# Performance work log

Measured on AMD Instinct MI355X. Metric: run time of the kernel, lower is better.

## Reference

```python
import jax, jax.numpy as jnp
import numpy as np

N = 25000        # nodes
E = 400000       # edges (avg degree 16)
F = 128          # num_features
NRBF = 20        # num_rbf_features
CUTOFF = 5.0


def setup_inputs() -> dict:
    key = jax.random.key(0)
    ks = jax.random.split(key, 9)
    node_scalar = jax.random.normal(ks[0], (N, F), jnp.float32)
    node_vector = jax.random.normal(ks[1], (N, F, 3), jnp.float32)
    dst = jax.random.randint(ks[2], (E,), 0, N)
    src = jax.random.randint(ks[3], (E,), 0, N)
    r = jax.random.normal(ks[4], (E, 3), jnp.float32) * 1.5
    d = jnp.clip(jnp.linalg.norm(r, axis=-1), 0.1, None)
    adj_matrix = jnp.concatenate(
        [dst[:, None].astype(jnp.float32), src[:, None].astype(jnp.float32), r, d[:, None]],
        axis=-1)  # [E, 6]
    s_in = 1.0 / np.sqrt(F)
    s_rbf = 1.0 / np.sqrt(NRBF)
    W1 = jax.random.normal(ks[5], (F, F), jnp.float32) * s_in
    b1 = jnp.zeros((F,), jnp.float32)
    W2 = jax.random.normal(ks[6], (F, 3 * F), jnp.float32) * s_in
    b2 = jnp.zeros((3 * F,), jnp.float32)
    Wr = jax.random.normal(ks[7], (NRBF, 3 * F), jnp.float32) * s_rbf
    br = jnp.zeros((3 * F,), jnp.float32)
    return dict(node_scalar=node_scalar, node_vector=node_vector, adj_matrix=adj_matrix,
                W1=W1, b1=b1, W2=W2, b2=b2, Wr=Wr, br=br)


def reference(node_scalar, node_vector, adj_matrix, W1, b1, W2, b2, Wr, br):
    # scalar message MLP: Linear -> SiLU -> Linear, [N, 3F]
    atom_scalar = jax.nn.silu(node_scalar @ W1 + b1) @ W2 + b2

    dst = adj_matrix[:, 0].astype(jnp.int32)
    src = adj_matrix[:, 1].astype(jnp.int32)
    r_ij = adj_matrix[:, 2:5]              # [E, 3]
    d = adj_matrix[:, 5]                   # [E]

    # sinc expansion: sin(d * n * pi / cutoff) / d, n = 1..NRBF -> [E, NRBF]
    n_vals = jnp.arange(1, NRBF + 1, dtype=jnp.float32)
    sinc = jnp.sin(d[:, None] * n_vals * jnp.pi / CUTOFF) / d[:, None]
    rbf = sinc @ Wr + br                   # [E, 3F]
    cut = jnp.where(d < CUTOFF, 0.5 * (jnp.cos(jnp.pi * d / CUTOFF) + 1.0), 0.0)
    w = rbf * cut[:, None]                 # [E, 3F]

    pre_split = atom_scalar[src] * w       # [E, 3F]
    s1, s2, s3 = jnp.split(pre_split, 3, axis=-1)  # each [E, F]

    r_hat = r_ij / d[:, None]              # [E, 3]
    # message_vector: [E, F, 3]
    message_vector = node_vector[src] * s1[:, :, None] + s3[:, :, None] * r_hat[:, None, :]

    delta_s = jnp.zeros_like(node_scalar).at[dst].add(s2)
    delta_v = jnp.zeros_like(node_vector).at[dst].add(message_vector)
    return node_scalar + delta_s, node_vector + delta_v
```

## Files before the change

kernel.cpp:

```cpp
#include <hip/hip_runtime.h>

#define FDIM 128
#define NRBF 20
constexpr float CUTOFF_F = 5.0f;
constexpr float PI_F = 3.14159265358979323846f;

typedef _Float16 h2 __attribute__((ext_vector_type(2)));

__device__ __forceinline__ uint packh(float a, float b) {
  union { _Float16 h[2]; uint u; } x;
  x.h[0] = (_Float16)a;
  x.h[1] = (_Float16)b;
  return x.u;
}
__device__ __forceinline__ float h_lo(uint w) {
  union { uint u; _Float16 h[2]; } x;
  x.u = w;
  return (float)x.h[0];
}
__device__ __forceinline__ float h_hi(uint w) {
  union { uint u; _Float16 h[2]; } x;
  x.u = w;
  return (float)x.h[1];
}
__device__ __forceinline__ ushort f2us(float f) {
  union { _Float16 h; ushort s; } x;
  x.h = (_Float16)f;
  return x.s;
}
__device__ __forceinline__ float dot2(uint cw, h2 w, float acc) {
#if __has_builtin(__builtin_amdgcn_fdot2)
  h2 c = __builtin_bit_cast(h2, cw);
  return __builtin_amdgcn_fdot2(c, w, acc, false);
#else
  return fmaf(h_hi(cw), (float)w[1], fmaf(h_lo(cw), (float)w[0], acc));
#endif
}

__global__ __launch_bounds__(256) void gemm_fused(
    const float* __restrict__ A, const float* __restrict__ W1,
    const float* __restrict__ b1, const float* __restrict__ W2,
    const float* __restrict__ b2, ushort* __restrict__ atomh, int M) {
  __shared__ float As[64][FDIM + 4];
  const int row0 = blockIdx.x * 64;
  const int t = threadIdx.x;
  const int tx = t & 15;
  const int ty = t >> 4;
  const int cl = tx * 8;
  const int r0 = ty * 4;

  for (int i = t; i < 64 * 32; i += 256) {
    int r = i >> 5;
    int cc = (i & 31) << 2;
    int gr = row0 + r;
    float4 v = make_float4(0.f, 0.f, 0.f, 0.f);
    if (gr < M) v = *(const float4*)&A[(size_t)gr * FDIM + cc];
    *(float4*)&As[r][cc] = v;
  }
  __syncthreads();

  float acc[4][8];
#pragma unroll
  for (int r = 0; r < 4; ++r)
#pragma unroll
    for (int c = 0; c < 8; ++c) acc[r][c] = 0.f;
#pragma unroll 4
  for (int k = 0; k < FDIM; ++k) {
    const float* wr = W1 + (size_t)k * FDIM + cl;
    float4 wa = *(const float4*)wr;
    float4 wb = *(const float4*)(wr + 4);
    float w[8] = {wa.x, wa.y, wa.z, wa.w, wb.x, wb.y, wb.z, wb.w};
    float a[4];
#pragma unroll
    for (int r = 0; r < 4; ++r) a[r] = As[r0 + r][k];
#pragma unroll
    for (int r = 0; r < 4; ++r)
#pragma unroll
      for (int c = 0; c < 8; ++c) acc[r][c] = fmaf(a[r], w[c], acc[r][c]);
  }
  float hv[4][8];
#pragma unroll
  for (int r = 0; r < 4; ++r)
#pragma unroll
    for (int c = 0; c < 8; ++c) {
      float x = acc[r][c] + b1[cl + c];
      hv[r][c] = x / (1.f + __expf(-x));
    }
  __syncthreads();
#pragma unroll
  for (int r = 0; r < 4; ++r)
#pragma unroll
    for (int c = 0; c < 8; ++c) As[r0 + r][cl + c] = hv[r][c];
  __syncthreads();

#pragma unroll 1
  for (int p = 0; p < 3; ++p) {
    const int c0 = p * 128 + cl;
#pragma unroll
    for (int r = 0; r < 4; ++r)
#pragma unroll
      for (int c = 0; c < 8; ++c) acc[r][c] = 0.f;
#pragma unroll 4
    for (int k = 0; k < FDIM; ++k) {
      const float* wr = W2 + (size_t)k * 384 + c0;
      float4 wa = *(const float4*)wr;
      float4 wb = *(const float4*)(wr + 4);
      float w[8] = {wa.x, wa.y, wa.z, wa.w, wb.x, wb.y, wb.z, wb.w};
      float a[4];
#pragma unroll
      for (int r = 0; r < 4; ++r) a[r] = As[r0 + r][k];
#pragma unroll
      for (int r = 0; r < 4; ++r)
#pragma unroll
        for (int c = 0; c < 8; ++c) acc[r][c] = fmaf(a[r], w[c], acc[r][c]);
    }
#pragma unroll
    for (int r = 0; r < 4; ++r) {
      int gr = row0 + r0 + r;
      if (gr >= M) continue;
      union { ushort s[8]; uint4 q; } pk;
#pragma unroll
      for (int c = 0; c < 8; ++c) pk.s[c] = f2us(acc[r][c] + b2[c0 + c]);
      *(uint4*)&atomh[(size_t)gr * 384 + c0] = pk.q;
    }
  }
}

__global__ __launch_bounds__(256) void pack_kernel(
    const ushort* __restrict__ atomh, const float* __restrict__ nvec,
    uint* __restrict__ bundle, int NF) {
  for (int i = blockIdx.x * blockDim.x + threadIdx.x; i < NF;
       i += gridDim.x * blockDim.x) {
    int n = i >> 7, j = i & 127;
    const ushort* ab = atomh + (size_t)n * 384;
    uint a0 = ab[j], a1 = ab[j + 128], a2 = ab[j + 256];
    const float* vb = nvec + (size_t)i * 3;
    uint* o = bundle + (size_t)i * 3;
    o[0] = a0 | (a1 << 16);
    o[1] = a2 | ((uint)f2us(vb[0]) << 16);
    o[2] = (uint)f2us(vb[1]) | ((uint)f2us(vb[2]) << 16);
  }
}

__global__ __launch_bounds__(256) void hist_kernel(const float* __restrict__ adj,
                                                   int* __restrict__ counts,
                                                   int E) {
  int e = blockIdx.x * blockDim.x + threadIdx.x;
  if (e < E) atomicAdd(&counts[(int)adj[(size_t)e * 6]], 1);
}

__global__ __launch_bounds__(1024) void scan_kernel(
    const int* __restrict__ counts, int* __restrict__ offs,
    int* __restrict__ cursor, int n) {
  __shared__ int part[1024];
  const int tid = threadIdx.x;
  const int CH = (n + 1023) >> 10;
  const int b = tid * CH;
  const int e = min(b + CH, n);
  int s = 0;
  for (int i = b; i < e; ++i) s += counts[i];
  part[tid] = s;
  __syncthreads();
  for (int off = 1; off < 1024; off <<= 1) {
    int v = (tid >= off) ? part[tid - off] : 0;
    __syncthreads();
    part[tid] += v;
    __syncthreads();
  }
  int run = part[tid] - s;
  if (tid == 0) offs[0] = 0;
  for (int i = b; i < e; ++i) {
    int c = counts[i];
    cursor[i] = run;
    run += c;
    offs[i + 1] = run;
  }
}

__global__ __launch_bounds__(256) void edge_prep(const float* __restrict__ adj,
                                                 int* __restrict__ cursor,
                                                 int* __restrict__ eids,
                                                 uint* __restrict__ rec, int E) {
  int e = blockIdx.x * blockDim.x + threadIdx.x;
  if (e >= E) return;
  const float* a = adj + (size_t)e * 6;
  int dst = (int)a[0];
  int src = (int)a[1];
  float rx = a[2], ry = a[3], rz = a[4], d = a[5];

  int p = atomicAdd(&cursor[dst], 1);
  eids[p] = e;

  float x = d * (PI_F / CUTOFF_F);
  float sx, cx;
  __sincosf(x, &sx, &cx);
  float invd = 1.f / d;
  float cut = (d < CUTOFF_F) ? 0.5f * (cx + 1.f) : 0.f;
  float sc = invd * cut;

  union { uint w[16]; uint4 q[4]; } R;
  R.w[0] = (uint)src;
  R.w[1] = packh(rx * invd, ry * invd);
  R.w[2] = packh(rz * invd, cut);
  float twoc = 2.f * cx;
  float sprev = 0.f, scur = sx;
  float c[NRBF];
#pragma unroll
  for (int n = 0; n < NRBF; ++n) {
    c[n] = scur * sc;
    float nxt = fmaf(twoc, scur, -sprev);
    sprev = scur;
    scur = nxt;
  }
#pragma unroll
  for (int m = 0; m < 10; ++m) R.w[3 + m] = packh(c[2 * m], c[2 * m + 1]);
  R.w[13] = 0;
  R.w[14] = 0;
  R.w[15] = 0;
  uint4* o = (uint4*)(rec + ((size_t)e << 4));
#pragma unroll
  for (int m = 0; m < 4; ++m) o[m] = R.q[m];
}

__global__ __launch_bounds__(128) void accum_kernel(
    const uint* __restrict__ rec, const uint* __restrict__ bundle,
    const float* __restrict__ nvec, const float* __restrict__ Wr,
    const float* __restrict__ br, const float* __restrict__ ns,
    const int* __restrict__ offs, const int* __restrict__ eids,
    float* __restrict__ out_s, float* __restrict__ out_v, int Nn) {
  const int j = threadIdx.x;

  h2 wp0[10], wp1[10], wp2[10];
#pragma unroll
  for (int m = 0; m < 10; ++m) {
    wp0[m] = h2{(_Float16)Wr[(2 * m) * 384 + j], (_Float16)Wr[(2 * m + 1) * 384 + j]};
    wp1[m] = h2{(_Float16)Wr[(2 * m) * 384 + 128 + j], (_Float16)Wr[(2 * m + 1) * 384 + 128 + j]};
    wp2[m] = h2{(_Float16)Wr[(2 * m) * 384 + 256 + j], (_Float16)Wr[(2 * m + 1) * 384 + 256 + j]};
  }
  const float brj0 = br[j], brj1 = br[j + 128], brj2 = br[j + 256];

  __shared__ int sh_e[128], sh_s[128];

#define EID(t) ((t) < 128 ? sh_s[(t)] : eids[beg + (t)])
#define LOADREC(R, t)                                                      \
  {                                                                        \
    int eu = __builtin_amdgcn_readfirstlane(EID(t));                       \
    const uint* p = rec + ((size_t)(uint)eu << 4);                         \
    _Pragma("unroll") for (int w_ = 0; w_ < 13; ++w_) R[w_] = p[w_];       \
  }
#define LOADB(B0, B1, B2, SRC)                                             \
  {                                                                        \
    const uint* p = bundle + ((size_t)(uint)(SRC) * FDIM + j) * 3;         \
    B0 = p[0];                                                             \
    B1 = p[1];                                                             \
    B2 = p[2];                                                             \
  }

  for (int d = blockIdx.x; d < Nn; d += gridDim.x) {
    const int beg = offs[d];
    const int cnt = offs[d + 1] - beg;
    const int m = cnt < 128 ? cnt : 128;
    if (j < m) sh_e[j] = eids[beg + j];
    __syncthreads();
    if (j < m) {
      int v = sh_e[j];
      int r = 0;
      for (int u = 0; u < m; ++u) r += (sh_e[u] < v);
      sh_s[r] = v;
    }
    __syncthreads();

    float acc_s = 0.f, av0 = 0.f, av1 = 0.f, av2 = 0.f;

    uint r_cur[13], r_nxt[13];
    uint b0 = 0, b1 = 0, b2 = 0;
    if (cnt > 0) LOADREC(r_cur, 0);
    if (cnt > 1) LOADREC(r_nxt, 1);
    if (cnt > 0) LOADB(b0, b1, b2, (int)r_cur[0]);

    for (int t = 0; t < cnt; ++t) {
      uint nb0 = 0, nb1 = 0, nb2 = 0;
      if (t + 1 < cnt) LOADB(nb0, nb1, nb2, (int)r_nxt[0]);
      uint r_n2[13];
      if (t + 2 < cnt) LOADREC(r_n2, t + 2);

      float rhx = h_lo(r_cur[1]), rhy = h_hi(r_cur[1]);
      float rhz = h_lo(r_cur[2]), cut = h_hi(r_cur[2]);
      float w0 = cut * brj0, w1 = cut * brj1, w2 = cut * brj2;
#pragma unroll
      for (int q = 0; q < 10; ++q) {
        w0 = dot2(r_cur[3 + q], wp0[q], w0);
        w1 = dot2(r_cur[3 + q], wp1[q], w1);
        w2 = dot2(r_cur[3 + q], wp2[q], w2);
      }
      float s1 = h_lo(b0) * w0;
      float s2 = h_hi(b0) * w1;
      float s3 = h_lo(b1) * w2;
      float pv0 = h_hi(b1), pv1 = h_lo(b2), pv2 = h_hi(b2);
      acc_s += s2;
      av0 = fmaf(pv0, s1, fmaf(s3, rhx, av0));
      av1 = fmaf(pv1, s1, fmaf(s3, rhy, av1));
      av2 = fmaf(pv2, s1, fmaf(s3, rhz, av2));

#pragma unroll
      for (int w_ = 0; w_ < 13; ++w_) {
        r_cur[w_] = r_nxt[w_];
        r_nxt[w_] = r_n2[w_];
      }
      b0 = nb0;
      b1 = nb1;
      b2 = nb2;
    }

    out_s[(size_t)d * FDIM + j] = ns[(size_t)d * FDIM + j] + acc_s;
    float* vo = out_v + (size_t)d * 384 + j * 3;
    const float* vi = nvec + (size_t)d * 384 + j * 3;
    vo[0] = vi[0] + av0;
    vo[1] = vi[1] + av1;
    vo[2] = vi[2] + av2;
  }
#undef EID
#undef LOADREC
#undef LOADB
}

extern "C" void kernel_launch(void* const* d_in, const int* in_sizes, int n_in,
                              void* d_out, int out_size, void* d_ws,
                              size_t ws_size, hipStream_t stream) {
  const float* node_scalar = (const float*)d_in[0];
  const float* node_vector = (const float*)d_in[1];
  const float* adj = (const float*)d_in[2];
  const float* W1 = (const float*)d_in[3];
  const float* b1 = (const float*)d_in[4];
  const float* W2 = (const float*)d_in[5];
  const float* b2 = (const float*)d_in[6];
  const float* Wr = (const float*)d_in[7];
  const float* br = (const float*)d_in[8];

  const int N = in_sizes[0] / FDIM;
  const int E = in_sizes[2] / 6;

  float* out = (float*)d_out;
  float* out_s = out;
  float* out_v = out + (size_t)N * FDIM;

  ushort* atomh = (ushort*)d_out;

  char* w = (char*)d_ws;
  uint* bundle = (uint*)w;
  size_t off = (size_t)N * FDIM * 12;
  uint* rec = (uint*)(w + off);
  off += (size_t)E * 64;
  int* counts = (int*)(w + off);
  int* offs = counts + N;
  int* cursor = offs + N + 1;
  int* eids = cursor + N;

  hipMemsetAsync(counts, 0, (size_t)N * sizeof(int), stream);
  hist_kernel<<<(E + 255) / 256, 256, 0, stream>>>(adj, counts, E);
  scan_kernel<<<1, 1024, 0, stream>>>(counts, offs, cursor, N);
  edge_prep<<<(E + 255) / 256, 256, 0, stream>>>(adj, cursor, eids, rec, E);

  gemm_fused<<<(N + 63) / 64, 256, 0, stream>>>(node_scalar, W1, b1, W2, b2,
                                                atomh, N);
  pack_kernel<<<2048, 256, 0, stream>>>(atomh, node_vector, bundle, N * FDIM);

  const int agrid = N < 4096 ? N : 4096;
  accum_kernel<<<agrid, 128, 0, stream>>>(rec, bundle, node_vector, Wr, br,
                                          node_scalar, offs, eids, out_s,
                                          out_v, N);
}
```

Before: 341.4 us.

## Split src out of edge record, deepen prefetch to three edges

Edge records shrink from 64 to 48 bytes. The src index moves to a separate array that is gathered into shared memory while edges are sorted, so the bundle gather no longer waits on the record load. The accumulation loop now prefetches three edges ahead instead of two and is unrolled by 2. The node_scalar and node_vector loads for the output are hoisted ahead of the loop. The trade-off is more registers per thread, which may lower occupancy, plus an extra srcs array write and read.

```diff
diff --git a/kernel.cpp b/kernel.cpp
--- a/kernel.cpp
+++ b/kernel.cpp
@@ -180,6 +180,7 @@
 __global__ __launch_bounds__(256) void edge_prep(const float* __restrict__ adj,
                                                  int* __restrict__ cursor,
                                                  int* __restrict__ eids,
+                                                 int* __restrict__ srcs,
                                                  uint* __restrict__ rec, int E) {
   int e = blockIdx.x * blockDim.x + threadIdx.x;
   if (e >= E) return;
@@ -190,6 +191,7 @@
 
   int p = atomicAdd(&cursor[dst], 1);
   eids[p] = e;
+  srcs[e] = src;
 
   float x = d * (PI_F / CUTOFF_F);
   float sx, cx;
@@ -198,10 +200,9 @@
   float cut = (d < CUTOFF_F) ? 0.5f * (cx + 1.f) : 0.f;
   float sc = invd * cut;
 
-  union { uint w[16]; uint4 q[4]; } R;
-  R.w[0] = (uint)src;
-  R.w[1] = packh(rx * invd, ry * invd);
-  R.w[2] = packh(rz * invd, cut);
+  union { uint w[12]; uint4 q[3]; } R;
+  R.w[0] = packh(rx * invd, ry * invd);
+  R.w[1] = packh(rz * invd, cut);
   float twoc = 2.f * cx;
   float sprev = 0.f, scur = sx;
   float c[NRBF];
@@ -213,22 +214,24 @@
     scur = nxt;
   }
 #pragma unroll
-  for (int m = 0; m < 10; ++m) R.w[3 + m] = packh(c[2 * m], c[2 * m + 1]);
-  R.w[13] = 0;
-  R.w[14] = 0;
-  R.w[15] = 0;
-  uint4* o = (uint4*)(rec + ((size_t)e << 4));
-#pragma unroll
-  for (int m = 0; m < 4; ++m) o[m] = R.q[m];
-}
+  for (int m = 0; m < 10; ++m) R.w[2 + m] = packh(c[2 * m], c[2 * m + 1]);
+  uint4* o = (uint4*)(rec + (size_t)e * 12);
+#pragma unroll
+  for (int m = 0; m < 3; ++m) o[m] = R.q[m];
+}
+
+struct Rec { uint w[12]; };
+struct Bun { uint b[3]; };
 
 __global__ __launch_bounds__(128) void accum_kernel(
-    const uint* __restrict__ rec, const uint* __restrict__ bundle,
-    const float* __restrict__ nvec, const float* __restrict__ Wr,
-    const float* __restrict__ br, const float* __restrict__ ns,
-    const int* __restrict__ offs, const int* __restrict__ eids,
-    float* __restrict__ out_s, float* __restrict__ out_v, int Nn) {
+    const uint* __restrict__ rec, const int* __restrict__ srcs,
+    const uint* __restrict__ bundle, const float* __restrict__ nvec,
+    const float* __restrict__ Wr, const float* __restrict__ br,
+    const float* __restrict__ ns, const int* __restrict__ offs,
+    const int* __restrict__ eids, float* __restrict__ out_s,
+    float* __restrict__ out_v, int Nn) {
   const int j = threadIdx.x;
+  const int j3 = j * 3;
 
   h2 wp0[10], wp1[10], wp2[10];
 #pragma unroll
@@ -239,27 +242,33 @@
   }
   const float brj0 = br[j], brj1 = br[j + 128], brj2 = br[j + 256];
 
-  __shared__ int sh_e[128], sh_s[128];
-
-#define EID(t) ((t) < 128 ? sh_s[(t)] : eids[beg + (t)])
-#define LOADREC(R, t)                                                      \
-  {                                                                        \
-    int eu = __builtin_amdgcn_readfirstlane(EID(t));                       \
-    const uint* p = rec + ((size_t)(uint)eu << 4);                         \
-    _Pragma("unroll") for (int w_ = 0; w_ < 13; ++w_) R[w_] = p[w_];       \
-  }
-#define LOADB(B0, B1, B2, SRC)                                             \
-  {                                                                        \
-    const uint* p = bundle + ((size_t)(uint)(SRC) * FDIM + j) * 3;         \
-    B0 = p[0];                                                             \
-    B1 = p[1];                                                             \
-    B2 = p[2];                                                             \
+  __shared__ int sh_e[128], sh_s[128], sh_src[128];
+
+#define EID_AT(t) ((t) < 128 ? sh_s[(t)] : eids[beg + (t)])
+#define SRC_AT(t) ((t) < 128 ? sh_src[(t)] : srcs[eids[beg + (t)]])
+#define LOADREC(R, t)                                                       \
+  {                                                                         \
+    int eu = __builtin_amdgcn_readfirstlane(EID_AT(t));                     \
+    const uint* p = rec + (size_t)(uint)eu * 12;                            \
+    _Pragma("unroll") for (int w_ = 0; w_ < 12; ++w_) (R).w[w_] = p[w_];    \
+  }
+#define LOADB(B, t)                                                         \
+  {                                                                         \
+    int su = __builtin_amdgcn_readfirstlane(SRC_AT(t));                     \
+    const uint* p = bundle + (size_t)(uint)su * 384 + j3;                   \
+    (B).b[0] = p[0];                                                        \
+    (B).b[1] = p[1];                                                        \
+    (B).b[2] = p[2];                                                        \
   }
 
   for (int d = blockIdx.x; d < Nn; d += gridDim.x) {
     const int beg = offs[d];
     const int cnt = offs[d + 1] - beg;
     const int m = cnt < 128 ? cnt : 128;
+    const float nsj = ns[(size_t)d * FDIM + j];
+    const float* vi = nvec + (size_t)d * 384 + j3;
+    const float vi0 = vi[0], vi1 = vi[1], vi2 = vi[2];
+
     if (j < m) sh_e[j] = eids[beg + j];
     __syncthreads();
     if (j < m) {
@@ -267,59 +276,54 @@
       int r = 0;
       for (int u = 0; u < m; ++u) r += (sh_e[u] < v);
       sh_s[r] = v;
+      sh_src[r] = srcs[v];
     }
     __syncthreads();
 
     float acc_s = 0.f, av0 = 0.f, av1 = 0.f, av2 = 0.f;
 
-    uint r_cur[13], r_nxt[13];
-    uint b0 = 0, b1 = 0, b2 = 0;
-    if (cnt > 0) LOADREC(r_cur, 0);
-    if (cnt > 1) LOADREC(r_nxt, 1);
-    if (cnt > 0) LOADB(b0, b1, b2, (int)r_cur[0]);
-
+    Rec R0 = {}, R1 = {}, R2 = {}, R3 = {};
+    Bun B0 = {}, B1 = {}, B2 = {}, B3 = {};
+    if (cnt > 0) { LOADB(B0, 0); LOADREC(R0, 0); }
+    if (cnt > 1) { LOADB(B1, 1); LOADREC(R1, 1); }
+    if (cnt > 2) { LOADB(B2, 2); LOADREC(R2, 2); }
+
+#pragma unroll 2
     for (int t = 0; t < cnt; ++t) {
-      uint nb0 = 0, nb1 = 0, nb2 = 0;
-      if (t + 1 < cnt) LOADB(nb0, nb1, nb2, (int)r_nxt[0]);
-      uint r_n2[13];
-      if (t + 2 < cnt) LOADREC(r_n2, t + 2);
-
-      float rhx = h_lo(r_cur[1]), rhy = h_hi(r_cur[1]);
-      float rhz = h_lo(r_cur[2]), cut = h_hi(r_cur[2]);
+      if (t + 3 < cnt) {
+        LOADB(B3, t + 3);
+        LOADREC(R3, t + 3);
+      }
+      float rhx = h_lo(R0.w[0]), rhy = h_hi(R0.w[0]);
+      float rhz = h_lo(R0.w[1]), cut = h_hi(R0.w[1]);
       float w0 = cut * brj0, w1 = cut * brj1, w2 = cut * brj2;
 #pragma unroll
       for (int q = 0; q < 10; ++q) {
-        w0 = dot2(r_cur[3 + q], wp0[q], w0);
-        w1 = dot2(r_cur[3 + q], wp1[q], w1);
-        w2 = dot2(r_cur[3 + q], wp2[q], w2);
+        w0 = dot2(R0.w[2 + q], wp0[q], w0);
+        w1 = dot2(R0.w[2 + q], wp1[q], w1);
+        w2 = dot2(R0.w[2 + q], wp2[q], w2);
       }
-      float s1 = h_lo(b0) * w0;
-      float s2 = h_hi(b0) * w1;
-      float s3 = h_lo(b1) * w2;
-      float pv0 = h_hi(b1), pv1 = h_lo(b2), pv2 = h_hi(b2);
+      float s1 = h_lo(B0.b[0]) * w0;
+      float s2 = h_hi(B0.b[0]) * w1;
+      float s3 = h_lo(B0.b[1]) * w2;
+      float pv0 = h_hi(B0.b[1]), pv1 = h_lo(B0.b[2]), pv2 = h_hi(B0.b[2]);
       acc_s += s2;
       av0 = fmaf(pv0, s1, fmaf(s3, rhx, av0));
       av1 = fmaf(pv1, s1, fmaf(s3, rhy, av1));
       av2 = fmaf(pv2, s1, fmaf(s3, rhz, av2));
 
-#pragma unroll
-      for (int w_ = 0; w_ < 13; ++w_) {
-        r_cur[w_] = r_nxt[w_];
-        r_nxt[w_] = r_n2[w_];
-      }
-      b0 = nb0;
-      b1 = nb1;
-      b2 = nb2;
-    }
-
-    out_s[(size_t)d * FDIM + j] = ns[(size_t)d * FDIM + j] + acc_s;
-    float* vo = out_v + (size_t)d * 384 + j * 3;
-    const float* vi = nvec + (size_t)d * 384 + j * 3;
-    vo[0] = vi[0] + av0;
-    vo[1] = vi[1] + av1;
-    vo[2] = vi[2] + av2;
-  }
-#undef EID
+      R0 = R1; R1 = R2; R2 = R3;
+      B0 = B1; B1 = B2; B2 = B3;
+    }
+
+    out_s[(size_t)d * FDIM + j] = nsj + acc_s;
+    float* vo = out_v + (size_t)d * 384 + j3;
+    vo[0] = vi0 + av0;
+    vo[1] = vi1 + av1;
+    vo[2] = vi2 + av2;
+  }
+#undef EID_AT
+#undef SRC_AT
 #undef LOADREC
 #undef LOADB
 }
@@ -350,7 +354,9 @@
   uint* bundle = (uint*)w;
   size_t off = (size_t)N * FDIM * 12;
   uint* rec = (uint*)(w + off);
-  off += (size_t)E * 64;
+  off += (size_t)E * 48;
+  int* srcs = (int*)(w + off);
+  off += (size_t)E * 4;
   int* counts = (int*)(w + off);
   int* offs = counts + N;
   int* cursor = offs + N + 1;
@@ -359,14 +365,14 @@
   hipMemsetAsync(counts, 0, (size_t)N * sizeof(int), stream);
   hist_kernel<<<(E + 255) / 256, 256, 0, stream>>>(adj, counts, E);
   scan_kernel<<<1, 1024, 0, stream>>>(counts, offs, cursor, N);
-  edge_prep<<<(E + 255) / 256, 256, 0, stream>>>(adj, cursor, eids, rec, E);
+  edge_prep<<<(E + 255) / 256, 256, 0, stream>>>(adj, cursor, eids, srcs, rec, E);
 
   gemm_fused<<<(N + 63) / 64, 256, 0, stream>>>(node_scalar, W1, b1, W2, b2,
                                                 atomh, N);
   pack_kernel<<<2048, 256, 0, stream>>>(atomh, node_vector, bundle, N * FDIM);
 
   const int agrid = N < 4096 ? N : 4096;
-  accum_kernel<<<agrid, 128, 0, stream>>>(rec, bundle, node_vector, Wr, br,
-                                          node_scalar, offs, eids, out_s,
+  accum_kernel<<<agrid, 128, 0, stream>>>(rec, srcs, bundle, node_vector, Wr,
+                                          br, node_scalar, offs, eids, out_s,
                                           out_v, N);
 }
```

Measured after the change: 370.4 us. 1.09x slower.

## Use fp16 MFMA for node MLP and fuse bundle packing into GEMM

Applied to the files above, without the earlier changes.

The scalar-FMA MLP GEMM is replaced by fp16 16x16x16 MFMA instructions, fed by weights converted once per call into fragment-ordered half buffers by a new small kernel. The GEMM epilogue now writes the packed bundle (atom scalars plus the fp16 node vector) directly, which removes the separate pack kernel and its intermediate atomh buffer round trip. Edge records shrink from 16 to 14 words to cut memory traffic, at the cost of misaligned 56-byte strides. Inputs and hidden activations are rounded to fp16 before the matmul, which lowers precision.

```diff
diff --git a/kernel.cpp b/kernel.cpp
--- a/kernel.cpp
+++ b/kernel.cpp
@@ -6,6 +6,8 @@
 constexpr float PI_F = 3.14159265358979323846f;
 
 typedef _Float16 h2 __attribute__((ext_vector_type(2)));
+typedef _Float16 half4 __attribute__((ext_vector_type(4)));
+typedef float f32x4 __attribute__((ext_vector_type(4)));
 
 __device__ __forceinline__ uint packh(float a, float b) {
   union { _Float16 h[2]; uint u; } x;
@@ -22,11 +24,6 @@
   union { uint u; _Float16 h[2]; } x;
   x.u = w;
   return (float)x.h[1];
-}
-__device__ __forceinline__ ushort f2us(float f) {
-  union { _Float16 h; ushort s; } x;
-  x.h = (_Float16)f;
-  return x.s;
 }
 __device__ __forceinline__ float dot2(uint cw, h2 w, float acc) {
 #if __has_builtin(__builtin_amdgcn_fdot2)
@@ -37,108 +34,112 @@
 #endif
 }
 
+__global__ __launch_bounds__(256) void wconv2(const float* __restrict__ W1,
+                                              const float* __restrict__ W2,
+                                              _Float16* __restrict__ w1h,
+                                              _Float16* __restrict__ w2h) {
+  int idx = blockIdx.x * blockDim.x + threadIdx.x;
+  const float* W;
+  _Float16* outp;
+  int NC, NCOLS, base;
+  if (idx < 8 * 8 * 256) {
+    W = W1; outp = w1h; NC = 8; NCOLS = 128; base = idx;
+  } else if (idx < 8 * 8 * 256 + 8 * 24 * 256) {
+    W = W2; outp = w2h; NC = 24; NCOLS = 384; base = idx - 8 * 8 * 256;
+  } else {
+    return;
+  }
+  int i = base & 3;
+  int l = (base >> 2) & 63;
+  int rem = base >> 8;
+  int c = rem % NC, s = rem / NC;
+  int k = s * 16 + ((l >> 4) & 3) * 4 + i;
+  int col = c * 16 + (l & 15);
+  outp[base] = (_Float16)W[(size_t)k * NCOLS + col];
+}
+
 __global__ __launch_bounds__(256) void gemm_fused(
-    const float* __restrict__ A, const float* __restrict__ W1,
-    const float* __restrict__ b1, const float* __restrict__ W2,
-    const float* __restrict__ b2, ushort* __restrict__ atomh, int M) {
-  __shared__ float As[64][FDIM + 4];
+    const float* __restrict__ A, const half4* __restrict__ w1h,
+    const float* __restrict__ b1, const half4* __restrict__ w2h,
+    const float* __restrict__ b2, const float* __restrict__ nvec,
+    uint* __restrict__ bundle, int M) {
+  __shared__ _Float16 Ah[64][136];
+  const int t = threadIdx.x;
+  const int w = t >> 6;
+  const int l = t & 63;
+  const int lr = l & 15, lg = (l >> 4) & 3;
   const int row0 = blockIdx.x * 64;
-  const int t = threadIdx.x;
-  const int tx = t & 15;
-  const int ty = t >> 4;
-  const int cl = tx * 8;
-  const int r0 = ty * 4;
 
   for (int i = t; i < 64 * 32; i += 256) {
-    int r = i >> 5;
-    int cc = (i & 31) << 2;
+    int r = i >> 5, c4 = (i & 31) << 2;
     int gr = row0 + r;
     float4 v = make_float4(0.f, 0.f, 0.f, 0.f);
-    if (gr < M) v = *(const float4*)&A[(size_t)gr * FDIM + cc];
-    *(float4*)&As[r][cc] = v;
+    if (gr < M) v = *(const float4*)&A[(size_t)gr * FDIM + c4];
+    half4 hv = {(_Float16)v.x, (_Float16)v.y, (_Float16)v.z, (_Float16)v.w};
+    *(half4*)&Ah[r][c4] = hv;
   }
   __syncthreads();
 
-  float acc[4][8];
-#pragma unroll
-  for (int r = 0; r < 4; ++r)
-#pragma unroll
-    for (int c = 0; c < 8; ++c) acc[r][c] = 0.f;
-#pragma unroll 4
-  for (int k = 0; k < FDIM; ++k) {
-    const float* wr = W1 + (size_t)k * FDIM + cl;
-    float4 wa = *(const float4*)wr;
-    float4 wb = *(const float4*)(wr + 4);
-    float w[8] = {wa.x, wa.y, wa.z, wa.w, wb.x, wb.y, wb.z, wb.w};
-    float a[4];
-#pragma unroll
-    for (int r = 0; r < 4; ++r) a[r] = As[r0 + r][k];
-#pragma unroll
-    for (int r = 0; r < 4; ++r)
-#pragma unroll
-      for (int c = 0; c < 8; ++c) acc[r][c] = fmaf(a[r], w[c], acc[r][c]);
-  }
-  float hv[4][8];
-#pragma unroll
-  for (int r = 0; r < 4; ++r)
+  half4 af[8];
+#pragma unroll
+  for (int s = 0; s < 8; ++s)
+    af[s] = *(const half4*)&Ah[16 * w + lr][s * 16 + lg * 4];
+
+  f32x4 acc1[8];
+#pragma unroll
+  for (int c = 0; c < 8; ++c) acc1[c] = {0.f, 0.f, 0.f, 0.f};
+#pragma unroll
+  for (int s = 0; s < 8; ++s) {
 #pragma unroll
     for (int c = 0; c < 8; ++c) {
-      float x = acc[r][c] + b1[cl + c];
-      hv[r][c] = x / (1.f + __expf(-x));
-    }
+      half4 bf = w1h[(s * 8 + c) * 64 + l];
+      acc1[c] = __builtin_amdgcn_mfma_f32_16x16x16f16(af[s], bf, acc1[c], 0, 0, 0);
+    }
+  }
   __syncthreads();
 #pragma unroll
-  for (int r = 0; r < 4; ++r)
-#pragma unroll
-    for (int c = 0; c < 8; ++c) As[r0 + r][cl + c] = hv[r][c];
+  for (int c = 0; c < 8; ++c) {
+    float bb = b1[c * 16 + lr];
+#pragma unroll
+    for (int r = 0; r < 4; ++r) {
+      float x = acc1[c][r] + bb;
+      x = x / (1.f + __expf(-x));
+      Ah[16 * w + lg * 4 + r][c * 16 + lr] = (_Float16)x;
+    }
+  }
   __syncthreads();
 
+  half4 hf[8];
+#pragma unroll
+  for (int s = 0; s < 8; ++s)
+    hf[s] = *(const half4*)&Ah[16 * w + lr][s * 16 + lg * 4];
+
 #pragma unroll 1
-  for (int p = 0; p < 3; ++p) {
-    const int c0 = p * 128 + cl;
-#pragma unroll
-    for (int r = 0; r < 4; ++r)
-#pragma unroll
-      for (int c = 0; c < 8; ++c) acc[r][c] = 0.f;
-#pragma unroll 4
-    for (int k = 0; k < FDIM; ++k) {
-      const float* wr = W2 + (size_t)k * 384 + c0;
-      float4 wa = *(const float4*)wr;
-      float4 wb = *(const float4*)(wr + 4);
-      float w[8] = {wa.x, wa.y, wa.z, wa.w, wb.x, wb.y, wb.z, wb.w};
-      float a[4];
-#pragma unroll
-      for (int r = 0; r < 4; ++r) a[r] = As[r0 + r][k];
-#pragma unroll
-      for (int r = 0; r < 4; ++r)
-#pragma unroll
-        for (int c = 0; c < 8; ++c) acc[r][c] = fmaf(a[r], w[c], acc[r][c]);
-    }
+  for (int cg = 0; cg < 8; ++cg) {
+    f32x4 a3[3];
+#pragma unroll
+    for (int p = 0; p < 3; ++p) a3[p] = {0.f, 0.f, 0.f, 0.f};
+#pragma unroll
+    for (int s = 0; s < 8; ++s) {
+#pragma unroll
+      for (int p = 0; p < 3; ++p) {
+        half4 bf = w2h[(s * 24 + cg + p * 8) * 64 + l];
+        a3[p] = __builtin_amdgcn_mfma_f32_16x16x16f16(hf[s], bf, a3[p], 0, 0, 0);
+      }
+    }
+    const int j = cg * 16 + lr;
+    const float bb0 = b2[j], bb1 = b2[j + 128], bb2 = b2[j + 256];
 #pragma unroll
     for (int r = 0; r < 4; ++r) {
-      int gr = row0 + r0 + r;
-      if (gr >= M) continue;
-      union { ushort s[8]; uint4 q; } pk;
-#pragma unroll
-      for (int c = 0; c < 8; ++c) pk.s[c] = f2us(acc[r][c] + b2[c0 + c]);
-      *(uint4*)&atomh[(size_t)gr * 384 + c0] = pk.q;
-    }
-  }
-}
-
-__global__ __launch_bounds__(256) void pack_kernel(
-    const ushort* __restrict__ atomh, const float* __restrict__ nvec,
-    uint* __restrict__ bundle, int NF) {
-  for (int i = blockIdx.x * blockDim.x + threadIdx.x; i < NF;
-       i += gridDim.x * blockDim.x) {
-    int n = i >> 7, j = i & 127;
-    const ushort* ab = atomh + (size_t)n * 384;
-    uint a0 = ab[j], a1 = ab[j + 128], a2 = ab[j + 256];
-    const float* vb = nvec + (size_t)i * 3;
-    uint* o = bundle + (size_t)i * 3;
-    o[0] = a0 | (a1 << 16);
-    o[1] = a2 | ((uint)f2us(vb[0]) << 16);
-    o[2] = (uint)f2us(vb[1]) | ((uint)f2us(vb[2]) << 16);
+      int n = row0 + 16 * w + lg * 4 + r;
+      if (n >= M) continue;
+      const float* vb = nvec + ((size_t)n * FDIM + j) * 3;
+      float v0 = vb[0], v1 = vb[1], v2 = vb[2];
+      uint* o = bundle + ((size_t)n * FDIM + j) * 3;
+      o[0] = packh(a3[0][r] + bb0, a3[1][r] + bb1);
+      o[1] = packh(a3[2][r] + bb2, v0);
+      o[2] = packh(v1, v2);
+    }
   }
 }
 
@@ -198,7 +199,7 @@
   float cut = (d < CUTOFF_F) ? 0.5f * (cx + 1.f) : 0.f;
   float sc = invd * cut;
 
-  union { uint w[16]; uint4 q[4]; } R;
+  union { uint w[14]; uint2 q[7]; } R;
   R.w[0] = (uint)src;
   R.w[1] = packh(rx * invd, ry * invd);
   R.w[2] = packh(rz * invd, cut);
@@ -215,11 +216,9 @@
 #pragma unroll
   for (int m = 0; m < 10; ++m) R.w[3 + m] = packh(c[2 * m], c[2 * m + 1]);
   R.w[13] = 0;
-  R.w[14] = 0;
-  R.w[15] = 0;
-  uint4* o = (uint4*)(rec + ((size_t)e << 4));
-#pragma unroll
-  for (int m = 0; m < 4; ++m) o[m] = R.q[m];
+  uint2* o = (uint2*)(rec + (size_t)e * 14);
+#pragma unroll
+  for (int m = 0; m < 7; ++m) o[m] = R.q[m];
 }
 
 __global__ __launch_bounds__(128) void accum_kernel(
@@ -245,12 +244,12 @@
 #define LOADREC(R, t)                                                      \
   {                                                                        \
     int eu = __builtin_amdgcn_readfirstlane(EID(t));                       \
-    const uint* p = rec + ((size_t)(uint)eu << 4);                         \
+    const uint* p = rec + (size_t)(uint)eu * 14;                           \
     _Pragma("unroll") for (int w_ = 0; w_ < 13; ++w_) R[w_] = p[w_];       \
   }
 #define LOADB(B0, B1, B2, SRC)                                             \
   {                                                                        \
-    const uint* p = bundle + ((size_t)(uint)(SRC) * FDIM + j) * 3;         \
+    const uint* p = bundle + ((size_t)(uint)(SRC)*FDIM + j) * 3;           \
     B0 = p[0];                                                             \
     B1 = p[1];                                                             \
     B2 = p[2];                                                             \
@@ -344,13 +343,15 @@
   float* out_s = out;
   float* out_v = out + (size_t)N * FDIM;
 
-  ushort* atomh = (ushort*)d_out;
-
   char* w = (char*)d_ws;
   uint* bundle = (uint*)w;
   size_t off = (size_t)N * FDIM * 12;
   uint* rec = (uint*)(w + off);
-  off += (size_t)E * 64;
+  off += (size_t)E * 56;
+  _Float16* w1h = (_Float16*)(w + off);
+  off += 8 * 8 * 256 * 2;
+  _Float16* w2h = (_Float16*)(w + off);
+  off += 8 * 24 * 256 * 2;
   int* counts = (int*)(w + off);
   int* offs = counts + N;
   int* cursor = offs + N + 1;
@@ -361,9 +362,11 @@
   scan_kernel<<<1, 1024, 0, stream>>>(counts, offs, cursor, N);
   edge_prep<<<(E + 255) / 256, 256, 0, stream>>>(adj, cursor, eids, rec, E);
 
-  gemm_fused<<<(N + 63) / 64, 256, 0, stream>>>(node_scalar, W1, b1, W2, b2,
-                                                atomh, N);
-  pack_kernel<<<2048, 256, 0, stream>>>(atomh, node_vector, bundle, N * FDIM);
+  wconv2<<<(8 * 8 * 256 + 8 * 24 * 256 + 255) / 256, 256, 0, stream>>>(
+      W1, W2, w1h, w2h);
+  gemm_fused<<<(N + 63) / 64, 256, 0, stream>>>(node_scalar, (const half4*)w1h,
+                                                b1, (const half4*)w2h, b2,
+                                                node_vector, bundle, N);
 
   const int agrid = N < 4096 ? N : 4096;
   accum_kernel<<<agrid, 128, 0, stream>>>(rec, bundle, node_vector, Wr, br,
```

New measurement: 300.3 us. 12.0% less time.
